# Optimization experiments

Hardware: AMD Instinct MI355X
Metric: run time of the kernel (lower is better)

The kernel has to match this reference:

```python
import jax, jax.numpy as jnp
import numpy as np

N_TOKENS = 50257  # vocab size (init kwarg)


def setup_inputs() -> dict:
    key = jax.random.key(0)
    # [batch, seq] int token ids in [0, N_TOKENS)
    inputs = jax.random.randint(key, (1024, 512), 0, N_TOKENS, dtype=jnp.int32)
    return {"inputs": inputs}


def reference(inputs) -> jnp.ndarray:
    # Faithful math: sum_j one_hot(inputs[b, j], N_TOKENS) -> token count histogram,
    # then drop token id 0 (padding). Implemented as a scatter-add instead of
    # materializing the [B, S, V] one-hot tensor.
    B, S = inputs.shape
    rows = jnp.arange(B, dtype=jnp.int32)[:, None]  # [B, 1] broadcast against [B, S]
    counts = jnp.zeros((B, N_TOKENS), dtype=jnp.float32)
    counts = counts.at[rows, inputs].add(jnp.float32(1.0))  # [B, V]
    return counts[:, 1:]  # drop token id 0, matches [:, 1:] in the original
```

## Files before the change

### kernel.cpp

```cpp
#include <hip/hip_runtime.h>
#include <hip/hip_bf16.h>


#define BATCH 1024
#define SEQ 512
#define VOCAB 50257
#define OUT_COLS (VOCAB - 1)

__global__ void bow_scatter_kernel(const int* __restrict__ tokens,
                                   float* __restrict__ out) {
    int idx = blockIdx.x * blockDim.x + threadIdx.x;
    if (idx >= BATCH * SEQ) return;
    int b = idx >> 9;
    int tok = tokens[idx];
    if (tok != 0) {
        atomicAdd(&out[(long long)b * OUT_COLS + (tok - 1)], 1.0f);
    }
}

extern "C" void kernel_launch(void* const* d_in, const int* in_sizes, int n_in,
                              void* d_out, int out_size, void* d_ws, size_t ws_size,
                              hipStream_t stream) {
    const int* tokens = (const int*)d_in[0];
    float* out = (float*)d_out;

    hipMemsetAsync(out, 0, (size_t)out_size * sizeof(float), stream);

    const int total = BATCH * SEQ;
    const int block = 256;
    const int grid = (total + block - 1) / block;
    bow_scatter_kernel<<<grid, block, 0, stream>>>(tokens, out);
}
```

Baseline: 217.7 us.

## Fuse zero-fill and histogram into per-row LDS-chunk kernel with vectorized stores

Replaces the memset plus global-atomic scatter with one kernel. Each block owns one batch row and an 8192-column vocab chunk. It builds the counts in a shared-memory histogram using LDS atomics, then writes the whole chunk, zeros included, with float4 stores. This removes the separate memset pass and the scattered global atomics, at the cost of re-reading each row's tokens once per chunk (7 times).

```diff
diff --git a/kernel.cpp b/kernel.cpp
--- a/kernel.cpp
+++ b/kernel.cpp
@@ -6,15 +6,37 @@
 #define SEQ 512
 #define VOCAB 50257
 #define OUT_COLS (VOCAB - 1)
+#define CHUNK 8192
+#define NBLK_PER_ROW ((OUT_COLS + CHUNK - 1) / CHUNK)
+#define BLOCK 256
 
-__global__ void bow_scatter_kernel(const int* __restrict__ tokens,
-                                   float* __restrict__ out) {
-    int idx = blockIdx.x * blockDim.x + threadIdx.x;
-    if (idx >= BATCH * SEQ) return;
-    int b = idx >> 9;
-    int tok = tokens[idx];
-    if (tok != 0) {
-        atomicAdd(&out[(long long)b * OUT_COLS + (tok - 1)], 1.0f);
+__global__ __launch_bounds__(BLOCK) void bow_fused_kernel(
+    const int* __restrict__ tokens, float* __restrict__ out) {
+    __shared__ unsigned int hist[CHUNK];
+
+    const int c0 = blockIdx.x * CHUNK;
+    const int b  = blockIdx.y;
+    const int t  = threadIdx.x;
+
+    #pragma unroll
+    for (int i = t; i < CHUNK; i += BLOCK) hist[i] = 0u;
+    __syncthreads();
+
+    const int2* trow = (const int2*)(tokens + b * SEQ);
+    int2 tk = trow[t];
+    unsigned int c;
+    c = (unsigned int)(tk.x - 1 - c0);
+    if (c < CHUNK) atomicAdd(&hist[c], 1u);
+    c = (unsigned int)(tk.y - 1 - c0);
+    if (c < CHUNK) atomicAdd(&hist[c], 1u);
+    __syncthreads();
+
+    float* orow = out + (size_t)b * OUT_COLS + c0;
+    const int ncols = min(CHUNK, OUT_COLS - c0);
+    for (int i = t * 4; i < ncols; i += BLOCK * 4) {
+        uint4 h = *(const uint4*)&hist[i];
+        float4 v = make_float4((float)h.x, (float)h.y, (float)h.z, (float)h.w);
+        *(float4*)(orow + i) = v;
     }
 }
 
@@ -24,10 +46,6 @@
     const int* tokens = (const int*)d_in[0];
     float* out = (float*)d_out;
 
-    hipMemsetAsync(out, 0, (size_t)out_size * sizeof(float), stream);
-
-    const int total = BATCH * SEQ;
-    const int block = 256;
-    const int grid = (total + block - 1) / block;
-    bow_scatter_kernel<<<grid, block, 0, stream>>>(tokens, out);
+    dim3 grid(NBLK_PER_ROW, BATCH);
+    bow_fused_kernel<<<grid, BLOCK, 0, stream>>>(tokens, out);
 }
```

Measured after the change: 198.2 us. -9.0%, faster.

## Build per-row histograms in shared memory and write output densely, dropping memset

Applied to the files above, without the earlier changes.

Replaces the global memset plus scattered global atomicAdd with one block per (row, vocab half). Each block builds a histogram in LDS using two 16-bit counters packed into each 32-bit word, then writes its half of the row once with vectorized float4 stores. This removes the separate zero-fill pass and the uncoalesced global atomics, so the output is written only once. The cost is about 50KB of LDS per block, which limits occupancy, and each block reads its row's tokens a second time.

```diff
diff --git a/kernel.cpp b/kernel.cpp
--- a/kernel.cpp
+++ b/kernel.cpp
@@ -6,15 +6,37 @@
 #define SEQ 512
 #define VOCAB 50257
 #define OUT_COLS (VOCAB - 1)
+#define HALF_BINS (OUT_COLS / 2)
+#define NWORDS (HALF_BINS / 2)
+#define BLOCK 512
 
-__global__ void bow_scatter_kernel(const int* __restrict__ tokens,
-                                   float* __restrict__ out) {
-    int idx = blockIdx.x * blockDim.x + threadIdx.x;
-    if (idx >= BATCH * SEQ) return;
-    int b = idx >> 9;
-    int tok = tokens[idx];
-    if (tok != 0) {
-        atomicAdd(&out[(long long)b * OUT_COLS + (tok - 1)], 1.0f);
+__global__ __launch_bounds__(BLOCK) void bow_row_kernel(
+    const int* __restrict__ tokens, float* __restrict__ out) {
+    __shared__ unsigned int packed[NWORDS];
+
+    const int half = blockIdx.x;
+    const int b    = blockIdx.y;
+    const int t    = threadIdx.x;
+    const int c0   = half * HALF_BINS;
+
+    const uint4 z = make_uint4(0u, 0u, 0u, 0u);
+    for (int i = t; i < NWORDS / 4; i += BLOCK) ((uint4*)packed)[i] = z;
+    __syncthreads();
+
+    {
+        int tok = tokens[b * SEQ + t];
+        unsigned int bin = (unsigned int)(tok - 1 - c0);
+        if (bin < HALF_BINS)
+            atomicAdd(&packed[bin >> 1], (bin & 1) ? 0x10000u : 1u);
+    }
+    __syncthreads();
+
+    float* orow = out + (size_t)b * OUT_COLS + c0;
+    for (int i = t * 4; i < HALF_BINS; i += BLOCK * 4) {
+        uint2 w = *(const uint2*)&packed[i >> 1];
+        float4 v = make_float4((float)(w.x & 0xffffu), (float)(w.x >> 16),
+                               (float)(w.y & 0xffffu), (float)(w.y >> 16));
+        *(float4*)(orow + i) = v;
     }
 }
 
@@ -24,10 +46,6 @@
     const int* tokens = (const int*)d_in[0];
     float* out = (float*)d_out;
 
-    hipMemsetAsync(out, 0, (size_t)out_size * sizeof(float), stream);
-
-    const int total = BATCH * SEQ;
-    const int block = 256;
-    const int grid = (total + block - 1) / block;
-    bow_scatter_kernel<<<grid, block, 0, stream>>>(tokens, out);
+    dim3 grid(2, BATCH);
+    bow_row_kernel<<<grid, BLOCK, 0, stream>>>(tokens, out);
 }
```

New measurement: 197.4 us. -9.3%, faster.
